# Optimization experiments

Hardware: AMD Instinct MI355X
Metric: run time of the kernel (lower is better)

Reference implementation:

```python
import jax, jax.numpy as jnp
import numpy as np

D_IN, D_OUT = 128, 128


def setup_inputs() -> dict:
    key = jax.random.key(0)
    ks = jax.random.split(key, 12)
    B = 262144
    g = 1.0 / np.sqrt(D_IN)
    gc = 1.0 / np.sqrt(D_IN + D_OUT)
    go = 1.0 / np.sqrt(D_OUT)
    return {
        "x": jax.random.normal(ks[0], (B, D_IN), jnp.float32),
        "h_prev": jax.random.normal(ks[1], (1, D_OUT), jnp.float32) * 0.1,
        "W_slow_w": jax.random.normal(ks[2], (D_OUT, D_IN), jnp.float32) * g,
        "W_slow_b": jnp.zeros((D_OUT,), jnp.float32),
        "W_fast_w": jnp.zeros((D_OUT, D_IN), jnp.float32),
        "Wi_w": jax.random.normal(ks[3], (D_OUT, D_IN), jnp.float32) * g,
        "Wi_b": jnp.zeros((D_OUT,), jnp.float32),
        "Wf_w": jax.random.normal(ks[4], (D_OUT, D_IN + D_OUT), jnp.float32) * gc,
        "Wf_b": jnp.zeros((D_OUT,), jnp.float32),
        "Wo_w": jax.random.normal(ks[5], (D_OUT, D_OUT), jnp.float32) * go,
        "Wo_b": jnp.zeros((D_OUT,), jnp.float32),
        "ln_g": jnp.ones((D_OUT,), jnp.float32),
        "ln_b": jnp.zeros((D_OUT,), jnp.float32),
    }


def _linear(x, w, b=None):
    y = x @ w.T
    return y if b is None else y + b


def _layernorm(x, g, b, eps=1e-5):
    mu = jnp.mean(x, axis=-1, keepdims=True)
    var = jnp.var(x, axis=-1, keepdims=True)
    return (x - mu) * jax.lax.rsqrt(var + eps) * g + b


def reference(x, h_prev, W_slow_w, W_slow_b, W_fast_w, Wi_w, Wi_b,
              Wf_w, Wf_b, Wo_w, Wo_b, ln_g, ln_b):
    B = x.shape[0]
    hp = jnp.broadcast_to(h_prev, (B, h_prev.shape[1]))  # [B, d_out]
    i_t = jax.nn.sigmoid(_linear(x, Wi_w, Wi_b))
    f_t = jax.nn.sigmoid(_linear(jnp.concatenate([x, hp], axis=1), Wf_w, Wf_b))
    h_slow = _linear(x, W_slow_w, W_slow_b)
    h_fast = _linear(x, W_fast_w)
    h_raw = i_t * (h_slow + h_fast) + f_t * hp
    o_t = jax.nn.sigmoid(_linear(h_raw, Wo_w, Wo_b))
    h_out = o_t * jnp.tanh(h_raw)
    return _layernorm(h_out, ln_g, ln_b)
```

## Files before the change

### kernel.cpp

```cpp
#include <hip/hip_runtime.h>
#include <hip/hip_bf16.h>
#include <hip/hip_fp16.h>


typedef __attribute__((ext_vector_type(8)))  short short8;
typedef __attribute__((ext_vector_type(16))) float f32x16;

__device__ __forceinline__ unsigned short f2bf(float f) {
    union { float f; unsigned u; } v; v.f = f;
    unsigned r = v.u + 0x7fffu + ((v.u >> 16) & 1u);
    return (unsigned short)(r >> 16);
}
__device__ __forceinline__ unsigned pk_bf16(float lo, float hi) {
    union { __hip_bfloat162 h; unsigned u; } c;
    c.h = __float22bfloat162_rn(make_float2(lo, hi));
    return c.u;
}
__device__ __forceinline__ unsigned pk_f16(float lo, float hi) {
    union { __half2 h; unsigned u; } c;
    c.h = __floats2half2_rn(lo, hi);
    return c.u;
}
__device__ __forceinline__ float lo_f16(unsigned u) {
    union { unsigned u; __half2 h; } c; c.u = u;
    return __low2float(c.h);
}
__device__ __forceinline__ float hi_f16(unsigned u) {
    union { unsigned u; __half2 h; } c; c.u = u;
    return __high2float(c.h);
}
__device__ __forceinline__ float bf2f(unsigned hs) {
    union { unsigned u; float f; } v; v.u = hs << 16;
    return v.f;
}
__device__ __forceinline__ float rcp_fast(float x) { return __builtin_amdgcn_rcpf(x); }
__device__ __forceinline__ float exp2_fast(float x) { return __builtin_amdgcn_exp2f(x); }
__device__ __forceinline__ float sigm(float x) {
    return rcp_fast(1.0f + exp2_fast(-1.4426950408889634f * x));
}
__device__ __forceinline__ float tanh_fast(float x) {
    return 1.0f - 2.0f * rcp_fast(1.0f + exp2_fast(2.8853900817779268f * x));
}
__device__ __forceinline__ f32x16 mfma_bf16(short8 a, short8 b, f32x16 c) {
    return __builtin_amdgcn_mfma_f32_32x32x16_bf16(a, b, c, 0, 0, 0);
}

#define SWZ(r) ((unsigned)(((r) & 15) << 4))

__global__ void prep_weights(const float* __restrict__ Wi_w,
                             const float* __restrict__ Wf_w,
                             const float* __restrict__ Ws_w,
                             const float* __restrict__ Wfast_w,
                             const float* __restrict__ Wo_w,
                             unsigned short* __restrict__ Wshuf) {
    int gid = blockIdx.x * 256 + threadIdx.x;
    int e    = gid & 7;
    int lane = (gid >> 3) & 63;
    int ks   = (gid >> 9) & 7;
    int t    = gid >> 12;
    int g = t >> 2, jg = t & 3;
    int row = jg * 32 + (lane & 31);
    int k   = ks * 16 + (lane >> 5) * 8 + e;
    float v;
    if (g == 0)      v = Wi_w[row * 128 + k];
    else if (g == 1) v = Wf_w[row * 256 + k];
    else if (g == 2) v = Ws_w[row * 128 + k] + Wfast_w[row * 128 + k];
    else             v = Wo_w[row * 128 + k];
    Wshuf[gid] = f2bf(v);
}

__global__ void prep_fbias(const float* __restrict__ Wf_w,
                           const float* __restrict__ Wf_b,
                           const float* __restrict__ hp,
                           float* __restrict__ fbias) {
    int j = threadIdx.x;
    float s = Wf_b[j];
    for (int k = 0; k < 128; ++k) s += Wf_w[j * 256 + 128 + k] * hp[k];
    fbias[j] = s;
}

__global__ __launch_bounds__(256, 2)
void cell_main(const float* __restrict__ x,
               const float* __restrict__ hp,
               const float* __restrict__ Wi_b,
               const float* __restrict__ Ws_b,
               const float* __restrict__ Wo_b,
               const float* __restrict__ ln_g,
               const float* __restrict__ ln_b,
               const unsigned short* __restrict__ Wshuf,
               const float* __restrict__ fbias,
               float* __restrict__ out) {
    const int tid  = threadIdx.x;
    const int lane = tid & 63;
    const int w    = tid >> 6;
    const int lm   = lane & 31;
    const int h    = lane >> 5;

    __shared__ __align__(16) char  xh[16384];
    __shared__ __align__(16) float prm[7 * 128];
    __shared__ __align__(16) float red[4][4][32][2];
    __shared__ __align__(16) float red2[64][2];

    const size_t row0 = (size_t)blockIdx.x * 64;

    {
        const float4* xb = (const float4*)(x + row0 * 128);
        #pragma unroll
        for (int it = 0; it < 8; ++it) {
            const int idx = it * 256 + tid;
            const float4 v = xb[idx];
            const int r = idx >> 5;
            const unsigned off = ((unsigned)(r * 256 + (idx & 31) * 8)) ^ SWZ(r);
            *(uint2*)(xh + off) = make_uint2(pk_bf16(v.x, v.y), pk_bf16(v.z, v.w));
        }
        if (tid < 224) {
            const int a = tid >> 5, e4 = (tid & 31) * 4;
            float4 v;
            switch (a) {
                case 0: v = *(const float4*)(Wi_b + e4); break;
                case 1: v = *(const float4*)(Ws_b + e4); break;
                case 2: v = *(const float4*)(fbias + e4); break;
                case 3: v = *(const float4*)(hp + e4); break;
                case 4: v = *(const float4*)(Wo_b + e4); break;
                case 5: v = *(const float4*)(ln_g + e4); break;
                default: v = *(const float4*)(ln_b + e4); break;
            }
            *(float4*)(prm + a * 128 + e4) = v;
        }
    }
    __syncthreads();

    auto LDXF = [&](int mt, int ks) -> short8 {
        const int r = mt * 32 + lm;
        const unsigned off = (unsigned)(r * 256) + (((unsigned)(ks * 32 + h * 16)) ^ SWZ(r));
        return *(const short8*)(xh + off);
    };
    const unsigned short* Wl = Wshuf + (size_t)lane * 8;
    auto WFG = [&](int g, int ks) -> short8 {
        return *(const short8*)(const void*)(Wl + (size_t)((g * 4 + w) * 8 + ks) * 512);
    };

    unsigned ik[16];
    #pragma unroll
    for (int mt = 0; mt < 2; ++mt) {
        f32x16 acc;
        #pragma unroll
        for (int e = 0; e < 16; ++e) acc[e] = 0.f;
        #pragma unroll
        for (int ks = 0; ks < 8; ++ks)
            acc = mfma_bf16(WFG(0, ks), LDXF(mt, ks), acc);
        #pragma unroll
        for (int q = 0; q < 4; ++q) {
            const int n0 = w * 32 + q * 8 + h * 4;
            const float4 bi = *(const float4*)(prm + 0 * 128 + n0);
            ik[mt*8+q*2+0] = pk_f16(sigm(acc[q*4+0] + bi.x), sigm(acc[q*4+1] + bi.y));
            ik[mt*8+q*2+1] = pk_f16(sigm(acc[q*4+2] + bi.z), sigm(acc[q*4+3] + bi.w));
        }
    }

    unsigned ppk[16];
    #pragma unroll
    for (int mt = 0; mt < 2; ++mt) {
        f32x16 acc;
        #pragma unroll
        for (int e = 0; e < 16; ++e) acc[e] = 0.f;
        #pragma unroll
        for (int ks = 0; ks < 8; ++ks)
            acc = mfma_bf16(WFG(2, ks), LDXF(mt, ks), acc);
        #pragma unroll
        for (int q = 0; q < 4; ++q) {
            const int n0 = w * 32 + q * 8 + h * 4;
            const float4 bs = *(const float4*)(prm + 1 * 128 + n0);
            const unsigned ia = ik[mt*8+q*2+0], ib = ik[mt*8+q*2+1];
            ppk[mt*8+q*2+0] = pk_f16(lo_f16(ia) * (acc[q*4+0] + bs.x),
                                     hi_f16(ia) * (acc[q*4+1] + bs.y));
            ppk[mt*8+q*2+1] = pk_f16(lo_f16(ib) * (acc[q*4+2] + bs.z),
                                     hi_f16(ib) * (acc[q*4+3] + bs.w));
        }
    }

    unsigned hpk[16];
    #pragma unroll
    for (int mt = 0; mt < 2; ++mt) {
        f32x16 acc;
        #pragma unroll
        for (int e = 0; e < 16; ++e) acc[e] = 0.f;
        #pragma unroll
        for (int ks = 0; ks < 8; ++ks)
            acc = mfma_bf16(WFG(1, ks), LDXF(mt, ks), acc);
        #pragma unroll
        for (int q = 0; q < 4; ++q) {
            const int n0 = w * 32 + q * 8 + h * 4;
            const float4 fb4 = *(const float4*)(prm + 2 * 128 + n0);
            const float4 hp4 = *(const float4*)(prm + 3 * 128 + n0);
            const unsigned pa = ppk[mt*8+q*2+0], pb = ppk[mt*8+q*2+1];
            hpk[mt*8+q*2+0] = pk_bf16(lo_f16(pa) + sigm(acc[q*4+0] + fb4.x) * hp4.x,
                                      hi_f16(pa) + sigm(acc[q*4+1] + fb4.y) * hp4.y);
            hpk[mt*8+q*2+1] = pk_bf16(lo_f16(pb) + sigm(acc[q*4+2] + fb4.z) * hp4.z,
                                      hi_f16(pb) + sigm(acc[q*4+3] + fb4.w) * hp4.w);
        }
    }
    __syncthreads();

    #pragma unroll
    for (int mt = 0; mt < 2; ++mt) {
        const int r = mt * 32 + lm;
        #pragma unroll
        for (int q = 0; q < 4; ++q) {
            const unsigned off = (unsigned)(r * 256)
                + (((unsigned)((w * 32 + q * 8 + h * 4) * 2)) ^ SWZ(r));
            *(uint2*)(xh + off) = make_uint2(hpk[mt*8+q*2+0], hpk[mt*8+q*2+1]);
        }
    }
    __syncthreads();

    unsigned opk[16];
    {
        float sums[2], ssqs[2];
        #pragma unroll
        for (int mt = 0; mt < 2; ++mt) {
            f32x16 acc;
            #pragma unroll
            for (int e = 0; e < 16; ++e) acc[e] = 0.f;
            #pragma unroll
            for (int ks = 0; ks < 8; ++ks)
                acc = mfma_bf16(WFG(3, ks), LDXF(mt, ks), acc);
            float sum = 0.f, ssq = 0.f;
            #pragma unroll
            for (int q = 0; q < 4; ++q) {
                const int n0 = w * 32 + q * 8 + h * 4;
                const float4 bo = *(const float4*)(prm + 4 * 128 + n0);
                const unsigned ha = hpk[mt*8+q*2+0], hb = hpk[mt*8+q*2+1];
                const float hv0 = sigm(acc[q*4+0] + bo.x) * tanh_fast(bf2f(ha & 0xffffu));
                const float hv1 = sigm(acc[q*4+1] + bo.y) * tanh_fast(bf2f(ha >> 16));
                const float hv2 = sigm(acc[q*4+2] + bo.z) * tanh_fast(bf2f(hb & 0xffffu));
                const float hv3 = sigm(acc[q*4+3] + bo.w) * tanh_fast(bf2f(hb >> 16));
                opk[mt*8+q*2+0] = pk_f16(hv0, hv1);
                opk[mt*8+q*2+1] = pk_f16(hv2, hv3);
                sum += hv0 + hv1 + hv2 + hv3;
                ssq += hv0*hv0 + hv1*hv1 + hv2*hv2 + hv3*hv3;
            }
            sum += __shfl_xor(sum, 32, 64);
            ssq += __shfl_xor(ssq, 32, 64);
            sums[mt] = sum; ssqs[mt] = ssq;
        }
        if (h == 0) {
            #pragma unroll
            for (int mt = 0; mt < 2; ++mt) {
                red[mt][w][lm][0] = sums[mt];
                red[mt][w][lm][1] = ssqs[mt];
            }
        }
    }
    __syncthreads();

    #pragma unroll
    for (int mt = 0; mt < 2; ++mt) {
        const int r = mt * 32 + lm;
        #pragma unroll
        for (int q = 0; q < 4; ++q) {
            const unsigned off = (unsigned)(r * 256)
                + (((unsigned)((w * 32 + q * 8 + h * 4) * 2)) ^ SWZ(r));
            *(uint2*)(xh + off) = make_uint2(opk[mt*8+q*2+0], opk[mt*8+q*2+1]);
        }
    }
    if (tid < 64) {
        const int mt = tid >> 5, l = tid & 31;
        float s = 0.f, q2 = 0.f;
        #pragma unroll
        for (int ww = 0; ww < 4; ++ww) {
            s  += red[mt][ww][l][0];
            q2 += red[mt][ww][l][1];
        }
        const float mean = s * (1.0f / 128.0f);
        const float var  = q2 * (1.0f / 128.0f) - mean * mean;
        red2[tid][0] = mean;
        red2[tid][1] = __builtin_amdgcn_rsqf(var + 1e-5f);
    }
    __syncthreads();

    float* ob = out + row0 * 128;
    #pragma unroll
    for (int it = 0; it < 8; ++it) {
        const int idx = it * 256 + tid;
        const int r = idx >> 5;
        const int c4 = (idx & 31) * 4;
        const unsigned off = (unsigned)(r * 256) + (((unsigned)(c4 * 2)) ^ SWZ(r));
        const uint2 hv = *(const uint2*)(xh + off);
        const float mean = red2[r][0], rstd = red2[r][1];
        const float4 g4 = *(const float4*)(prm + 5 * 128 + c4);
        const float4 b4 = *(const float4*)(prm + 6 * 128 + c4);
        float4 rr;
        rr.x = (lo_f16(hv.x) - mean) * rstd * g4.x + b4.x;
        rr.y = (hi_f16(hv.x) - mean) * rstd * g4.y + b4.y;
        rr.z = (lo_f16(hv.y) - mean) * rstd * g4.z + b4.z;
        rr.w = (hi_f16(hv.y) - mean) * rstd * g4.w + b4.w;
        *(float4*)(ob + (size_t)idx * 4) = rr;
    }
}

extern "C" void kernel_launch(void* const* d_in, const int* in_sizes, int n_in,
                              void* d_out, int out_size, void* d_ws, size_t ws_size,
                              hipStream_t stream) {
    const float* x      = (const float*)d_in[0];
    const float* h_prev = (const float*)d_in[1];
    const float* Ws_w   = (const float*)d_in[2];
    const float* Ws_b   = (const float*)d_in[3];
    const float* Wfast  = (const float*)d_in[4];
    const float* Wi_w   = (const float*)d_in[5];
    const float* Wi_b   = (const float*)d_in[6];
    const float* Wf_w   = (const float*)d_in[7];
    const float* Wf_b   = (const float*)d_in[8];
    const float* Wo_w   = (const float*)d_in[9];
    const float* Wo_b   = (const float*)d_in[10];
    const float* ln_g   = (const float*)d_in[11];
    const float* ln_b   = (const float*)d_in[12];

    unsigned short* Wshuf = (unsigned short*)d_ws;
    float*          fb    = (float*)(Wshuf + 65536);

    prep_weights<<<256, 256, 0, stream>>>(Wi_w, Wf_w, Ws_w, Wfast, Wo_w, Wshuf);
    prep_fbias<<<1, 128, 0, stream>>>(Wf_w, Wf_b, h_prev, fb);

    const int B = in_sizes[0] / 128;
    const int blocks = B / 64;
    cell_main<<<blocks, 256, 0, stream>>>(x, h_prev, Wi_b, Ws_b, Wo_b,
                                          ln_g, ln_b, Wshuf, fb,
                                          (float*)d_out);
}
```

Before: 92.47 us.

## Halve rows per block and fuse three gate GEMMs into one k-loop

Each block now handles 32 rows instead of 64, which doubles the grid size and halves LDS per block, and the launch bound is raised to 3 blocks per SM. The input, slow and forget gate MFMAs share one pass over k, so each x fragment is loaded once for three accumulators, and the intermediate packed f16 registers are dropped. The goal is more resident waves and better latency hiding for this memory-bound kernel. In exchange, each block loads weights from global/L2 for half as many rows, three accumulators raise register pressure, and the tighter launch bound may cause spills.

```diff
diff --git a/kernel.cpp b/kernel.cpp
--- a/kernel.cpp
+++ b/kernel.cpp
@@ -79,7 +79,7 @@
     fbias[j] = s;
 }
 
-__global__ __launch_bounds__(256, 2)
+__global__ __launch_bounds__(256, 3)
 void cell_main(const float* __restrict__ x,
                const float* __restrict__ hp,
                const float* __restrict__ Wi_b,
@@ -96,17 +96,17 @@
     const int lm   = lane & 31;
     const int h    = lane >> 5;
 
-    __shared__ __align__(16) char  xh[16384];
+    __shared__ __align__(16) char  xh[8192];
     __shared__ __align__(16) float prm[7 * 128];
-    __shared__ __align__(16) float red[4][4][32][2];
-    __shared__ __align__(16) float red2[64][2];
-
-    const size_t row0 = (size_t)blockIdx.x * 64;
+    __shared__ __align__(16) float red[4][32][2];
+    __shared__ __align__(16) float red2[32][2];
+
+    const size_t row0 = (size_t)blockIdx.x * 32;
 
     {
         const float4* xb = (const float4*)(x + row0 * 128);
         #pragma unroll
-        for (int it = 0; it < 8; ++it) {
+        for (int it = 0; it < 4; ++it) {
             const int idx = it * 256 + tid;
             const float4 v = xb[idx];
             const int r = idx >> 5;
@@ -130,9 +130,9 @@
     }
     __syncthreads();
 
-    auto LDXF = [&](int mt, int ks) -> short8 {
-        const int r = mt * 32 + lm;
-        const unsigned off = (unsigned)(r * 256) + (((unsigned)(ks * 32 + h * 16)) ^ SWZ(r));
+    auto LDXF = [&](int ks) -> short8 {
+        const unsigned off = (unsigned)(lm * 256)
+            + (((unsigned)(ks * 32 + h * 16)) ^ SWZ(lm));
         return *(const short8*)(xh + off);
     };
     const unsigned short* Wl = Wshuf + (size_t)lane * 8;
@@ -140,137 +140,88 @@
         return *(const short8*)(const void*)(Wl + (size_t)((g * 4 + w) * 8 + ks) * 512);
     };
 
-    unsigned ik[16];
-    #pragma unroll
-    for (int mt = 0; mt < 2; ++mt) {
-        f32x16 acc;
-        #pragma unroll
-        for (int e = 0; e < 16; ++e) acc[e] = 0.f;
-        #pragma unroll
-        for (int ks = 0; ks < 8; ++ks)
-            acc = mfma_bf16(WFG(0, ks), LDXF(mt, ks), acc);
+    unsigned hpk[8];
+    {
+        f32x16 ai, as_, af;
+        #pragma unroll
+        for (int e = 0; e < 16; ++e) { ai[e] = 0.f; as_[e] = 0.f; af[e] = 0.f; }
+        #pragma unroll
+        for (int ks = 0; ks < 8; ++ks) {
+            const short8 xv = LDXF(ks);
+            ai  = mfma_bf16(WFG(0, ks), xv, ai);
+            as_ = mfma_bf16(WFG(2, ks), xv, as_);
+            af  = mfma_bf16(WFG(1, ks), xv, af);
+        }
         #pragma unroll
         for (int q = 0; q < 4; ++q) {
             const int n0 = w * 32 + q * 8 + h * 4;
-            const float4 bi = *(const float4*)(prm + 0 * 128 + n0);
-            ik[mt*8+q*2+0] = pk_f16(sigm(acc[q*4+0] + bi.x), sigm(acc[q*4+1] + bi.y));
-            ik[mt*8+q*2+1] = pk_f16(sigm(acc[q*4+2] + bi.z), sigm(acc[q*4+3] + bi.w));
-        }
-    }
-
-    unsigned ppk[16];
+            const float4 bi  = *(const float4*)(prm + 0 * 128 + n0);
+            const float4 bs  = *(const float4*)(prm + 1 * 128 + n0);
+            const float4 fb4 = *(const float4*)(prm + 2 * 128 + n0);
+            const float4 hp4 = *(const float4*)(prm + 3 * 128 + n0);
+            const float h0 = sigm(ai[q*4+0] + bi.x) * (as_[q*4+0] + bs.x)
+                           + sigm(af[q*4+0] + fb4.x) * hp4.x;
+            const float h1 = sigm(ai[q*4+1] + bi.y) * (as_[q*4+1] + bs.y)
+                           + sigm(af[q*4+1] + fb4.y) * hp4.y;
+            const float h2 = sigm(ai[q*4+2] + bi.z) * (as_[q*4+2] + bs.z)
+                           + sigm(af[q*4+2] + fb4.z) * hp4.z;
+            const float h3 = sigm(ai[q*4+3] + bi.w) * (as_[q*4+3] + bs.w)
+                           + sigm(af[q*4+3] + fb4.w) * hp4.w;
+            hpk[q*2+0] = pk_bf16(h0, h1);
+            hpk[q*2+1] = pk_bf16(h2, h3);
+        }
+    }
+    __syncthreads();
+
     #pragma unroll
-    for (int mt = 0; mt < 2; ++mt) {
+    for (int q = 0; q < 4; ++q) {
+        const unsigned off = (unsigned)(lm * 256)
+            + (((unsigned)((w * 32 + q * 8 + h * 4) * 2)) ^ SWZ(lm));
+        *(uint2*)(xh + off) = make_uint2(hpk[q*2+0], hpk[q*2+1]);
+    }
+    __syncthreads();
+
+    unsigned opk[8];
+    {
         f32x16 acc;
         #pragma unroll
         for (int e = 0; e < 16; ++e) acc[e] = 0.f;
         #pragma unroll
         for (int ks = 0; ks < 8; ++ks)
-            acc = mfma_bf16(WFG(2, ks), LDXF(mt, ks), acc);
+            acc = mfma_bf16(WFG(3, ks), LDXF(ks), acc);
+        float sum = 0.f, ssq = 0.f;
         #pragma unroll
         for (int q = 0; q < 4; ++q) {
             const int n0 = w * 32 + q * 8 + h * 4;
-            const float4 bs = *(const float4*)(prm + 1 * 128 + n0);
-            const unsigned ia = ik[mt*8+q*2+0], ib = ik[mt*8+q*2+1];
-            ppk[mt*8+q*2+0] = pk_f16(lo_f16(ia) * (acc[q*4+0] + bs.x),
-                                     hi_f16(ia) * (acc[q*4+1] + bs.y));
-            ppk[mt*8+q*2+1] = pk_f16(lo_f16(ib) * (acc[q*4+2] + bs.z),
-                                     hi_f16(ib) * (acc[q*4+3] + bs.w));
-        }
-    }
-
-    unsigned hpk[16];
+            const float4 bo = *(const float4*)(prm + 4 * 128 + n0);
+            const unsigned ha = hpk[q*2+0], hb = hpk[q*2+1];
+            const float hv0 = sigm(acc[q*4+0] + bo.x) * tanh_fast(bf2f(ha & 0xffffu));
+            const float hv1 = sigm(acc[q*4+1] + bo.y) * tanh_fast(bf2f(ha >> 16));
+            const float hv2 = sigm(acc[q*4+2] + bo.z) * tanh_fast(bf2f(hb & 0xffffu));
+            const float hv3 = sigm(acc[q*4+3] + bo.w) * tanh_fast(bf2f(hb >> 16));
+            opk[q*2+0] = pk_f16(hv0, hv1);
+            opk[q*2+1] = pk_f16(hv2, hv3);
+            sum += hv0 + hv1 + hv2 + hv3;
+            ssq += hv0*hv0 + hv1*hv1 + hv2*hv2 + hv3*hv3;
+        }
+        sum += __shfl_xor(sum, 32, 64);
+        ssq += __shfl_xor(ssq, 32, 64);
+        if (h == 0) { red[w][lm][0] = sum; red[w][lm][1] = ssq; }
+    }
+    __syncthreads();
+
     #pragma unroll
-    for (int mt = 0; mt < 2; ++mt) {
-        f32x16 acc;
-        #pragma unroll
-        for (int e = 0; e < 16; ++e) acc[e] = 0.f;
-        #pragma unroll
-        for (int ks = 0; ks < 8; ++ks)
-            acc = mfma_bf16(WFG(1, ks), LDXF(mt, ks), acc);
-        #pragma unroll
-        for (int q = 0; q < 4; ++q) {
-            const int n0 = w * 32 + q * 8 + h * 4;
-            const float4 fb4 = *(const float4*)(prm + 2 * 128 + n0);
-            const float4 hp4 = *(const float4*)(prm + 3 * 128 + n0);
-            const unsigned pa = ppk[mt*8+q*2+0], pb = ppk[mt*8+q*2+1];
-            hpk[mt*8+q*2+0] = pk_bf16(lo_f16(pa) + sigm(acc[q*4+0] + fb4.x) * hp4.x,
-                                      hi_f16(pa) + sigm(acc[q*4+1] + fb4.y) * hp4.y);
-            hpk[mt*8+q*2+1] = pk_bf16(lo_f16(pb) + sigm(acc[q*4+2] + fb4.z) * hp4.z,
-                                      hi_f16(pb) + sigm(acc[q*4+3] + fb4.w) * hp4.w);
-        }
-    }
-    __syncthreads();
-
-    #pragma unroll
-    for (int mt = 0; mt < 2; ++mt) {
-        const int r = mt * 32 + lm;
-        #pragma unroll
-        for (int q = 0; q < 4; ++q) {
-            const unsigned off = (unsigned)(r * 256)
-                + (((unsigned)((w * 32 + q * 8 + h * 4) * 2)) ^ SWZ(r));
-            *(uint2*)(xh + off) = make_uint2(hpk[mt*8+q*2+0], hpk[mt*8+q*2+1]);
-        }
-    }
-    __syncthreads();
-
-    unsigned opk[16];
-    {
-        float sums[2], ssqs[2];
-        #pragma unroll
-        for (int mt = 0; mt < 2; ++mt) {
-            f32x16 acc;
-            #pragma unroll
-            for (int e = 0; e < 16; ++e) acc[e] = 0.f;
-            #pragma unroll
-            for (int ks = 0; ks < 8; ++ks)
-                acc = mfma_bf16(WFG(3, ks), LDXF(mt, ks), acc);
-            float sum = 0.f, ssq = 0.f;
-            #pragma unroll
-            for (int q = 0; q < 4; ++q) {
-                const int n0 = w * 32 + q * 8 + h * 4;
-                const float4 bo = *(const float4*)(prm + 4 * 128 + n0);
-                const unsigned ha = hpk[mt*8+q*2+0], hb = hpk[mt*8+q*2+1];
-                const float hv0 = sigm(acc[q*4+0] + bo.x) * tanh_fast(bf2f(ha & 0xffffu));
-                const float hv1 = sigm(acc[q*4+1] + bo.y) * tanh_fast(bf2f(ha >> 16));
-                const float hv2 = sigm(acc[q*4+2] + bo.z) * tanh_fast(bf2f(hb & 0xffffu));
-                const float hv3 = sigm(acc[q*4+3] + bo.w) * tanh_fast(bf2f(hb >> 16));
-                opk[mt*8+q*2+0] = pk_f16(hv0, hv1);
-                opk[mt*8+q*2+1] = pk_f16(hv2, hv3);
-                sum += hv0 + hv1 + hv2 + hv3;
-                ssq += hv0*hv0 + hv1*hv1 + hv2*hv2 + hv3*hv3;
-            }
-            sum += __shfl_xor(sum, 32, 64);
-            ssq += __shfl_xor(ssq, 32, 64);
-            sums[mt] = sum; ssqs[mt] = ssq;
-        }
-        if (h == 0) {
-            #pragma unroll
-            for (int mt = 0; mt < 2; ++mt) {
-                red[mt][w][lm][0] = sums[mt];
-                red[mt][w][lm][1] = ssqs[mt];
-            }
-        }
-    }
-    __syncthreads();
-
-    #pragma unroll
-    for (int mt = 0; mt < 2; ++mt) {
-        const int r = mt * 32 + lm;
-        #pragma unroll
-        for (int q = 0; q < 4; ++q) {
-            const unsigned off = (unsigned)(r * 256)
-                + (((unsigned)((w * 32 + q * 8 + h * 4) * 2)) ^ SWZ(r));
-            *(uint2*)(xh + off) = make_uint2(opk[mt*8+q*2+0], opk[mt*8+q*2+1]);
-        }
-    }
-    if (tid < 64) {
-        const int mt = tid >> 5, l = tid & 31;
+    for (int q = 0; q < 4; ++q) {
+        const unsigned off = (unsigned)(lm * 256)
+            + (((unsigned)((w * 32 + q * 8 + h * 4) * 2)) ^ SWZ(lm));
+        *(uint2*)(xh + off) = make_uint2(opk[q*2+0], opk[q*2+1]);
+    }
+    if (tid < 32) {
         float s = 0.f, q2 = 0.f;
         #pragma unroll
         for (int ww = 0; ww < 4; ++ww) {
-            s  += red[mt][ww][l][0];
-            q2 += red[mt][ww][l][1];
+            s  += red[ww][tid][0];
+            q2 += red[ww][tid][1];
         }
         const float mean = s * (1.0f / 128.0f);
         const float var  = q2 * (1.0f / 128.0f) - mean * mean;
@@ -281,7 +232,7 @@
 
     float* ob = out + row0 * 128;
     #pragma unroll
-    for (int it = 0; it < 8; ++it) {
+    for (int it = 0; it < 4; ++it) {
         const int idx = it * 256 + tid;
         const int r = idx >> 5;
         const int c4 = (idx & 31) * 4;
@@ -323,7 +274,7 @@
     prep_fbias<<<1, 128, 0, stream>>>(Wf_w, Wf_b, h_prev, fb);
 
     const int B = in_sizes[0] / 128;
-    const int blocks = B / 64;
+    const int blocks = B / 32;
     cell_main<<<blocks, 256, 0, stream>>>(x, h_prev, Wi_b, Ws_b, Wo_b,
                                           ln_g, ln_b, Wshuf, fb,
                                           (float*)d_out);
```

After: 117.5 us. +27.1%, slower.
